# Kernel optimization log

Measured on AMD Instinct MI355X. Metric: run time of the kernel, lower is better.

The kernel has to match this reference:

```python
import jax, jax.numpy as jnp
import numpy as np

ALPHA, BETA, INIT_P = 100.0, 1000.0, 2.0
K_NEIGHBORS = 24


def index_points(pts, idx):
    # pts: [B,N,C], idx: [B,...] int -> [B,...,C]
    B = pts.shape[0]
    b = jnp.arange(B).reshape((B,) + (1,) * (idx.ndim - 1))
    return pts[b, idx]


def fps(xyz, m):
    # furthest point sampling, deterministic start at index 0. xyz: [B,N,3]
    B, N, _ = xyz.shape
    def step(carry, _):
        dist, far = carry
        centroid = xyz[jnp.arange(B), far]              # [B,3]
        d = jnp.sum((xyz - centroid[:, None, :]) ** 2, -1)
        dist = jnp.minimum(dist, d)
        nxt = jnp.argmax(dist, -1).astype(jnp.int32)
        return (dist, nxt), far
    init = (jnp.full((B, N), 1e10, xyz.dtype), jnp.zeros((B,), jnp.int32))
    _, idx = jax.lax.scan(step, init, None, length=m)
    return idx.T                                        # [B,m]


def knn_indices(k, xyz, centers):
    # squared distances [B,G,N], k smallest
    d = (jnp.sum(centers ** 2, -1)[..., None]
         - 2.0 * jnp.einsum('bgc,bnc->bgn', centers, xyz)
         + jnp.sum(xyz ** 2, -1)[:, None, :])
    _, idx = jax.lax.top_k(-d, k)
    return idx                                          # [B,G,K]


def normalize(x, ref):
    # torch: mean = ref.unsqueeze(-2); std over ALL elements of (x-mean), ddof=1
    d = x - ref[..., None, :]
    std = jnp.std(d, ddof=1)
    return d / (std + 1e-5)


def fourier_map(t, Bmat):
    # t: [B,7,G,K]; Bmat: [7, C//2] (already includes scale) -> [B,C,G,K]
    x = jnp.transpose(t, (0, 2, 3, 1))                  # [B,G,K,7]
    proj = 2.0 * jnp.pi * (x @ Bmat)                    # [B,G,K,C/2]
    f = jnp.concatenate([jnp.sin(proj), jnp.cos(proj)], -1)
    f = jnp.sign(f) * jnp.abs(f) ** 5
    return jnp.transpose(f, (0, 3, 1, 2))


def tr_embed(my_dim, t):
    # t: [B,3,G,K] -> [B,my_dim,G,K]
    B, C, G, K = t.shape
    F = my_dim // (2 * C)
    dim_embed = ALPHA ** (jnp.arange(F, dtype=t.dtype) / F)
    div = BETA * t[..., None] / dim_embed               # [B,3,G,K,F]
    pe = jnp.stack([jnp.sin(div), jnp.cos(div)], -1).reshape(B, C, G, K, 2 * F)
    pe = jnp.transpose(pe, (0, 1, 4, 2, 3)).reshape(B, my_dim, G, K)
    return pe


def lga(lc_xyz, lc_x, knn_xyz, knn_x, Bmat):
    B, G, K, C = knn_x.shape
    knn_x = normalize(knn_x, lc_x)
    knn_xyz = normalize(knn_xyz, lc_xyz)
    lc_rep = jnp.transpose(jnp.broadcast_to(lc_xyz[:, :, None, :], (B, G, K, 3)), (0, 3, 1, 2))
    knn_xyz_t = jnp.transpose(knn_xyz, (0, 3, 1, 2))    # [B,3,G,K]
    knn_x_t = jnp.transpose(knn_x, (0, 3, 1, 2))        # [B,C,G,K]
    cross = jnp.cross(knn_xyz_t, lc_rep, axis=1)
    dot = jnp.sum(knn_xyz_t * lc_rep, 1, keepdims=True)
    emb_in = jnp.concatenate([knn_xyz_t, cross, dot], 1)  # [B,7,G,K]
    emb = fourier_map(emb_in, Bmat)                       # [B,C,G,K]
    knn_x_w = jnp.concatenate([knn_x_t, emb], 1)          # [B,2C,G,K]
    pe = tr_embed(2 * C, knn_xyz_t) + tr_embed(2 * C, lc_rep)
    return (knn_x_w + pe) * pe


def k_anp(x):
    # x: [B,2C,G,K], data-dependent p-norm attention over K
    std = jnp.std(x, axis=-1, ddof=1, keepdims=True)
    p = jax.lax.stop_gradient(INIT_P + jnp.log1p(std.mean()))  # torch uses .item()
    norm = jnp.sum(jnp.abs(x) ** p, -1, keepdims=True) ** (1.0 / p)
    lc = norm / (norm + 1e-8)
    e = jnp.exp(lc)
    return (x * e).mean(-1) / e.mean(-1)                # [B,2C,G]


def bn_gelu(x, gamma, beta):
    # BatchNorm1d in training mode (batch stats, biased var) + exact GELU
    mean = x.mean((0, 2), keepdims=True)
    var = ((x - mean) ** 2).mean((0, 2), keepdims=True)
    y = (x - mean) / jnp.sqrt(var + 1e-5) * gamma[None, :, None] + beta[None, :, None]
    return jax.nn.gelu(y, approximate=False)


def stage(xyz, x, group_num, Bmat, gamma, beta):
    # xyz: [B,N,3]; x: [B,C,N]
    feats = jnp.transpose(x, (0, 2, 1))
    fi = fps(xyz, group_num)
    lc_xyz = index_points(xyz, fi)
    lc_x = index_points(feats, fi)
    ki = knn_indices(K_NEIGHBORS, xyz, lc_xyz)
    knn_xyz = index_points(xyz, ki)
    knn_x = index_points(feats, ki)
    w = lga(lc_xyz, lc_x, knn_xyz, knn_x, Bmat)
    pooled = k_anp(w) + w.mean(-1)                      # [B,2C,G]
    return lc_xyz, bn_gelu(pooled, gamma, beta)


def setup_inputs() -> dict:
    key = jax.random.key(0)
    k1, k2, k3, k4 = jax.random.split(key, 4)
    B, N, C0 = 4, 4096, 72
    return {
        'xyz': jax.random.uniform(k1, (B, N, 3), jnp.float32),
        'x': jax.random.normal(k2, (B, C0, N), jnp.float32),
        'fourier_B0': jax.random.normal(k3, (7, C0 // 2), jnp.float32) * 50.0,
        'fourier_B1': jax.random.normal(k4, (7, C0), jnp.float32) * 50.0,
        'bn_gamma0': jnp.ones((2 * C0,), jnp.float32),
        'bn_beta0': jnp.zeros((2 * C0,), jnp.float32),
        'bn_gamma1': jnp.ones((4 * C0,), jnp.float32),
        'bn_beta1': jnp.zeros((4 * C0,), jnp.float32),
    }


def reference(xyz, x, fourier_B0, fourier_B1, bn_gamma0, bn_beta0, bn_gamma1, bn_beta1):
    N = xyz.shape[1]
    xyz, x = stage(xyz, x, N // 2, fourier_B0, bn_gamma0, bn_beta0)   # -> [B,144,2048]
    xyz, x = stage(xyz, x, N // 4, fourier_B1, bn_gamma1, bn_beta1)   # -> [B,288,1024]
    return x
```

## Files before the change

kernel.cpp:

```cpp
#include <hip/hip_runtime.h>
#include <math.h>

#define KNB 24

typedef float v2f __attribute__((ext_vector_type(2)));

template<int CTRL>
__device__ __forceinline__ float dppmax(float v) {
    int t = __builtin_amdgcn_update_dpp(0, __float_as_int(v), CTRL, 0xf, 0xf, true);
    return fmaxf(v, __int_as_float(t));
}
template<int CTRL>
__device__ __forceinline__ unsigned dppmaxu(unsigned v) {
    unsigned t = (unsigned)__builtin_amdgcn_update_dpp(0, (int)v, CTRL, 0xf, 0xf, true);
    return v > t ? v : t;
}

template<int NPT, int NWAVE>
__global__ __launch_bounds__(64 * NWAVE) void k_fps_tr(const float* __restrict__ xyz,
                                                       int* __restrict__ fi,
                                                       int N, int M,
                                                       const float* __restrict__ x0,
                                                       float* __restrict__ feats,
                                                       int C, int NT, int nT, int cT) {
#pragma clang fp contract(off)
    const int NP2 = NPT / 2;
    const int tid = threadIdx.x;
    extern __shared__ char smc[];

    if ((int)blockIdx.x >= gridDim.x - 0 && false) return;

    if ((int)blockIdx.x >= (int)(gridDim.x) ) return;

    if ((int)blockIdx.x >= (int)0 && (int)blockIdx.x >= (int)( 0) && false) return;

    if ((int)blockIdx.x >= (int)( (int)gridDim.x - nT * cT * 4 ) && (int)blockIdx.x >= 4) {
        int bid = blockIdx.x - 4;
        int tilesPerB = nT * cT;
        int b = bid / tilesPerB;
        int t2 = bid - b * tilesPerB;
        int cTile = t2 / nT;
        int nTile = t2 - cTile * nT;
        int tx = tid & 31, ty = tid >> 5;
        float* tile = (float*)smc;
#pragma unroll
        for (int k = 0; k < 4; ++k) {
            int c = cTile * 32 + ty + k * 8, n = nTile * 32 + tx;
            if (c < C && n < NT) tile[(ty + k * 8) * 33 + tx] = x0[((size_t)b * C + c) * NT + n];
        }
        __syncthreads();
#pragma unroll
        for (int k = 0; k < 4; ++k) {
            int n = nTile * 32 + ty + k * 8, c = cTile * 32 + tx;
            if (c < C && n < NT) feats[((size_t)b * NT + n) * C + c] = tile[tx * 33 + ty + k * 8];
        }
        return;
    }

    const int b = blockIdx.x;
    const int lane = tid & 63;
    const int wid = tid >> 6;
    unsigned long long* keys = (unsigned long long*)smc;
    int* fi_lds = (int*)(smc + 2 * NWAVE * 8);
    size_t poff = ((size_t)(2 * NWAVE * 8) + (size_t)M * 4 + 15) & ~(size_t)15;
    float4* pts = (float4*)(smc + poff);

    const float* p = xyz + (size_t)b * N * 3;
    for (int i = tid; i < N; i += 64 * NWAVE)
        pts[i] = make_float4(p[i*3], p[i*3+1], p[i*3+2], 0.0f);
    __syncthreads();

    const int base = tid * NPT;
    v2f rx[NP2], ry[NP2], rz[NP2], dist[NP2];
#pragma unroll
    for (int j = 0; j < NP2; ++j) {
        float4 a = pts[base + 2*j];
        float4 c = pts[base + 2*j + 1];
        rx[j] = (v2f){a.x, c.x}; ry[j] = (v2f){a.y, c.y}; rz[j] = (v2f){a.z, c.z};
        dist[j] = (v2f){1e10f, 1e10f};
    }

    int far = 0;
    float4 cpt = pts[0];
    float cx = cpt.x, cy = cpt.y, cz = cpt.z;
    for (int it = 0; it < M; ++it) {
        if (tid == 0) fi_lds[it] = far;
        v2f cx2 = (v2f){cx, cx}, cy2 = (v2f){cy, cy}, cz2 = (v2f){cz, cz};
        v2f bv2 = (v2f){-1.0f, -1.0f};
#pragma unroll
        for (int j = 0; j < NP2; ++j) {
            v2f dx = rx[j] - cx2, dy = ry[j] - cy2, dz = rz[j] - cz2;
            v2f d = (dx*dx + dy*dy) + dz*dz;
            v2f dd = __builtin_elementwise_min(dist[j], d);
            dist[j] = dd;
            bv2 = __builtin_elementwise_max(bv2, dd);
        }
        float bv = fmaxf(bv2.x, bv2.y);
        int bi = 0;
#pragma unroll
        for (int j = NP2 - 1; j >= 0; --j) {
            if (dist[j].y == bv) bi = base + 2*j + 1;
            if (dist[j].x == bv) bi = base + 2*j;
        }
        float r = bv;
        r = dppmax<0x111>(r); r = dppmax<0x112>(r);
        r = dppmax<0x114>(r); r = dppmax<0x118>(r);
        r = dppmax<0x142>(r); r = dppmax<0x143>(r);
        float wmax = __int_as_float(__builtin_amdgcn_readlane(__float_as_int(r), 63));
        unsigned long long mask = __ballot(bv == wmax);
        int src = __builtin_ctzll(mask);
        int wbi = __builtin_amdgcn_readlane(bi, src);
        unsigned long long key =
            ((unsigned long long)__float_as_uint(wmax) << 32) | (unsigned)(~wbi);
        if (lane == 0) keys[(it & 1) * NWAVE + wid] = key;
        __syncthreads();
        unsigned long long k0 = keys[(it & 1) * NWAVE + 0];
#pragma unroll
        for (int w = 1; w < NWAVE; ++w) {
            unsigned long long kw = keys[(it & 1) * NWAVE + w];
            if (kw > k0) k0 = kw;
        }
        far = (int)(~(unsigned)k0);
        float4 c = pts[far];
        cx = c.x; cy = c.y; cz = c.z;
    }
    __syncthreads();
    for (int i = tid; i < M; i += 64 * NWAVE) fi[b * M + i] = fi_lds[i];
}

template<int NPT>
__global__ __launch_bounds__(256) void k_knn_t(const float* __restrict__ xyz,
                                               const float* __restrict__ feats,
                                               const int* __restrict__ fi,
                                               float* __restrict__ lc_xyz,
                                               float* __restrict__ lc_x,
                                               int* __restrict__ ki,
                                               double* __restrict__ part,
                                               int B, int N, int G, int C, int identity) {
#pragma clang fp contract(off)
    int bg = blockIdx.x; int b = bg / G; int g = bg % G;
    int idx = identity ? g : fi[bg];
    const int tid = threadIdx.x;
    const int lane = tid & 63;
    const int wid = tid >> 6;
    __shared__ unsigned long long keys[2][4];
    __shared__ int kis[KNB];
    __shared__ float cfeat[144];
    const float* p = xyz + (size_t)b * N * 3;
    float cx = p[idx*3], cy = p[idx*3+1], cz = p[idx*3+2];
    if (tid < 3) lc_xyz[(size_t)bg * 3 + tid] = p[idx*3 + tid];
    for (int c = tid; c < C; c += 256) {
        float v = feats[((size_t)b * N + idx) * C + c];
        lc_x[(size_t)bg * C + c] = v;
        cfeat[c] = v;
    }
    float cc = (cx*cx + cy*cy) + cz*cz;
    const int base = tid * NPT;
    float dist[NPT];
#pragma unroll
    for (int j = 0; j < NPT; ++j) {
        float x0 = p[(base+j)*3], x1 = p[(base+j)*3+1], x2 = p[(base+j)*3+2];
        float xx = (x0*x0 + x1*x1) + x2*x2;
        float dt = (cx*x0 + cy*x1) + cz*x2;
        dist[j] = (cc - 2.0f*dt) + xx;
    }
    for (int kk = 0; kk < KNB; ++kk) {
        float bv = 1e30f;
#pragma unroll
        for (int j = 0; j < NPT; ++j) bv = fminf(bv, dist[j]);
        int lj = 0;
#pragma unroll
        for (int j = NPT - 1; j >= 0; --j) if (dist[j] == bv) lj = j;
        unsigned ub = ~__float_as_uint(bv);
        unsigned r = ub;
        r = dppmaxu<0x111>(r); r = dppmaxu<0x112>(r);
        r = dppmaxu<0x114>(r); r = dppmaxu<0x118>(r);
        r = dppmaxu<0x142>(r); r = dppmaxu<0x143>(r);
        unsigned uwin = (unsigned)__builtin_amdgcn_readlane((int)r, 63);
        unsigned long long mask = __ballot(ub == uwin);
        int src = __builtin_ctzll(mask);
        int gi = __builtin_amdgcn_readlane(base + lj, src);
        unsigned long long key = ((unsigned long long)uwin << 32) | (unsigned)(~gi);
        if (lane == 0) keys[kk & 1][wid] = key;
        __syncthreads();
        unsigned long long k0 = keys[kk & 1][0];
#pragma unroll
        for (int w = 1; w < 4; ++w) {
            unsigned long long kw = keys[kk & 1][w];
            if (kw > k0) k0 = kw;
        }
        int win = (int)(~(unsigned)k0);
        if (tid == 0) kis[kk] = win;
        if (win >= base && win < base + NPT) {
            int wj = win - base;
#pragma unroll
            for (int j = 0; j < NPT; ++j) if (j == wj) dist[j] = 1e30f;
        }
    }
    __syncthreads();
    if (tid < KNB) ki[(size_t)bg * KNB + tid] = kis[tid];
    double s = 0.0, s2 = 0.0, s3 = 0.0, s4 = 0.0;
    for (int i = tid; i < KNB * C; i += 256) {
        int k = i / C, c = i - k * C;
        float d = feats[((size_t)b * N + kis[k]) * C + c] - cfeat[c];
        s += (double)d; s2 += (double)d * (double)d;
    }
    if (tid < KNB * 3) {
        int k = tid / 3, c = tid - k * 3;
        float ctr = (c == 0) ? cx : ((c == 1) ? cy : cz);
        float d = p[kis[k] * 3 + c] - ctr;
        s3 += (double)d; s4 += (double)d * (double)d;
    }
    for (int off = 32; off > 0; off >>= 1) {
        s += __shfl_down(s, off); s2 += __shfl_down(s2, off);
        s3 += __shfl_down(s3, off); s4 += __shfl_down(s4, off);
    }
    __shared__ double sw[4][4];
    if ((tid & 63) == 0) {
        sw[wid][0] = s; sw[wid][1] = s2; sw[wid][2] = s3; sw[wid][3] = s4;
    }
    __syncthreads();
    if (tid == 0) {
        double t0 = 0.0, t1 = 0.0, t2 = 0.0, t3 = 0.0;
        for (int w = 0; w < 4; ++w) {
            t0 += sw[w][0]; t1 += sw[w][1]; t2 += sw[w][2]; t3 += sw[w][3];
        }
        double* q = part + (size_t)bg * 4;
        q[0] = t0; q[1] = t1; q[2] = t2; q[3] = t3;
    }
}

__global__ __launch_bounds__(1024) void k_reduce(const double* __restrict__ part,
                                                 double* __restrict__ acc, int n) {
    double s0 = 0.0, s1 = 0.0, s2 = 0.0, s3 = 0.0;
    for (int i = threadIdx.x; i < n; i += 1024) {
        const double* q = part + (size_t)i * 4;
        s0 += q[0]; s1 += q[1]; s2 += q[2]; s3 += q[3];
    }
    for (int off = 32; off > 0; off >>= 1) {
        s0 += __shfl_down(s0, off); s1 += __shfl_down(s1, off);
        s2 += __shfl_down(s2, off); s3 += __shfl_down(s3, off);
    }
    __shared__ double sw[16][4];
    int wid = threadIdx.x >> 6;
    if ((threadIdx.x & 63) == 0) {
        sw[wid][0] = s0; sw[wid][1] = s1; sw[wid][2] = s2; sw[wid][3] = s3;
    }
    __syncthreads();
    if (threadIdx.x == 0) {
        double t0 = 0.0, t1 = 0.0, t2 = 0.0, t3 = 0.0;
        for (int w = 0; w < 16; ++w) {
            t0 += sw[w][0]; t1 += sw[w][1]; t2 += sw[w][2]; t3 += sw[w][3];
        }
        acc[0] = t0; acc[1] = t1; acc[2] = t2; acc[3] = t3;
    }
}

__global__ __launch_bounds__(256) void k_feature(
    const float* __restrict__ xyz, const float* __restrict__ feats,
    const float* __restrict__ lc_xyz, const float* __restrict__ lc_x,
    const int* __restrict__ ki, const float* __restrict__ Bmat,
    const double* __restrict__ accp, float* __restrict__ pooled,
    int B, int N, int G, int C, double nx, double nz)
{
    int bg = blockIdx.x; int b = bg / G; int g = bg % G;
    int tid = threadIdx.x;
    int C2 = C >> 1;
    int Cout = 2 * C;
    int F = C / 3;
    extern __shared__ float sm[];
    float* t7    = sm;
    float* sxyzn = t7 + KNB * 7;
    int*   kidx  = (int*)(sxyzn + KNB * 3);
    float* semb  = (float*)(kidx + KNB);
    float* sfeat = semb + KNB * C;

    double a0 = accp[0], a1 = accp[1], a2 = accp[2], a3 = accp[3];
    double vx = (a1 - a0 * a0 / nx) / (nx - 1.0);
    float invx = 1.0f / (sqrtf((float)vx) + 1e-5f);
    double vz = (a3 - a2 * a2 / nz) / (nz - 1.0);
    float invz = 1.0f / (sqrtf((float)vz) + 1e-5f);

    float l0 = lc_xyz[(size_t)bg*3], l1 = lc_xyz[(size_t)bg*3+1], l2 = lc_xyz[(size_t)bg*3+2];

    if (tid < KNB) {
        int idx = ki[(size_t)bg * KNB + tid];
        kidx[tid] = idx;
        const float* q = xyz + ((size_t)b * N + idx) * 3;
        float a0f = (q[0]-l0)*invz, a1f = (q[1]-l1)*invz, a2f = (q[2]-l2)*invz;
        float c0 = a1f*l2 - a2f*l1;
        float c1 = a2f*l0 - a0f*l2;
        float c2 = a0f*l1 - a1f*l0;
        float dt = (a0f*l0 + a1f*l1) + a2f*l2;
        float* tp = t7 + tid * 7;
        tp[0]=a0f; tp[1]=a1f; tp[2]=a2f; tp[3]=c0; tp[4]=c1; tp[5]=c2; tp[6]=dt;
        sxyzn[tid*3]=a0f; sxyzn[tid*3+1]=a1f; sxyzn[tid*3+2]=a2f;
    }
    __syncthreads();
    for (int i = tid; i < KNB * C; i += blockDim.x) {
        int k = i / C, c = i - k * C;
        sfeat[i] = feats[((size_t)b * N + kidx[k]) * C + c];
    }
    const float TWO_PI = 6.2831854820251465f;
    for (int i = tid; i < KNB * C2; i += blockDim.x) {
        int k = i / C2, m2 = i % C2;
        const float* tp = t7 + k * 7;
        float s = 0.0f;
        for (int j = 0; j < 7; ++j) s += tp[j] * Bmat[j * C2 + m2];
        float pr = TWO_PI * s;
        float sn, cs;
        __sincosf(pr, &sn, &cs);
        float sn2 = sn*sn, cs2 = cs*cs;
        semb[k*C + m2]      = sn2*sn2*sn;
        semb[k*C + C2 + m2] = cs2*cs2*cs;
    }
    __syncthreads();
    for (int m = tid; m < Cout; m += blockDim.x) {
        int c3 = m / (2 * F);
        int r  = m % (2 * F);
        int f  = r >> 1;
        int trig = r & 1;
        float de = __powf(100.0f, (float)f / (float)F);
        float rde = 1000.0f / de;
        float lv = (c3 == 0) ? l0 : ((c3 == 1) ? l1 : l2);
        float a2v = lv * rde;
        float pe2 = trig ? __cosf(a2v) : __sinf(a2v);
        float lfm = (m < C) ? lc_x[(size_t)bg * C + m] : 0.0f;
        float acc = 0.0f;
        for (int k = 0; k < KNB; ++k) {
            float v;
            if (m < C) {
                v = (sfeat[k * C + m] - lfm) * invx;
            } else {
                v = semb[k * C + (m - C)];
            }
            float a1v = sxyzn[k*3 + c3] * rde;
            float pe1 = trig ? __cosf(a1v) : __sinf(a1v);
            float pe = pe1 + pe2;
            acc += (v + pe) * pe;
        }
        float mean = acc / 24.0f;
        pooled[((size_t)b * Cout + m) * G + g] = 2.0f * mean;
    }
}

__global__ __launch_bounds__(256) void k_bn(const float* __restrict__ pooled,
                                            const float* __restrict__ gamma,
                                            const float* __restrict__ beta,
                                            float* __restrict__ out,
                                            int B, int Cout, int G, int transposed) {
    int m = blockIdx.x;
    double s = 0.0, s2 = 0.0;
    for (int i = threadIdx.x; i < B * G; i += 256) {
        int b = i / G, g = i % G;
        float v = pooled[((size_t)b * Cout + m) * G + g];
        s += (double)v; s2 += (double)v * (double)v;
    }
    for (int off = 32; off > 0; off >>= 1) { s += __shfl_down(s, off); s2 += __shfl_down(s2, off); }
    __shared__ double sw[4], sw2[4];
    __shared__ float smv[2];
    int wid = threadIdx.x >> 6;
    if ((threadIdx.x & 63) == 0) { sw[wid] = s; sw2[wid] = s2; }
    __syncthreads();
    if (threadIdx.x == 0) {
        double ts = sw[0] + sw[1] + sw[2] + sw[3];
        double ts2 = sw2[0] + sw2[1] + sw2[2] + sw2[3];
        double n = (double)(B * G);
        double mean = ts / n;
        double var = ts2 / n - mean * mean;
        smv[0] = (float)mean; smv[1] = (float)var;
    }
    __syncthreads();
    float mean = smv[0], var = smv[1];
    float ga = gamma[m], be = beta[m];
    for (int i = threadIdx.x; i < B * G; i += 256) {
        int b = i / G, g = i % G;
        float v = pooled[((size_t)b * Cout + m) * G + g];
        float y = (v - mean) / sqrtf(var + 1e-5f) * ga + be;
        float ge = 0.5f * y * (1.0f + erff(y / 1.4142135381698608f));
        if (transposed) out[((size_t)b * G + g) * Cout + m] = ge;
        else            out[((size_t)b * Cout + m) * G + g] = ge;
    }
}

extern "C" void kernel_launch(void* const* d_in, const int* in_sizes, int n_in,
                              void* d_out, int out_size, void* d_ws, size_t ws_size,
                              hipStream_t stream) {
    const int B = 4, N1 = 4096, C0 = 72, G1 = 2048, Co1 = 144;
    const int N2 = 2048, C1 = 144, G2 = 1024, Co2 = 288;

    const float* xyz = (const float*)d_in[0];
    const float* x0  = (const float*)d_in[1];
    const float* B0  = (const float*)d_in[2];
    const float* B1  = (const float*)d_in[3];
    const float* g0  = (const float*)d_in[4];
    const float* be0 = (const float*)d_in[5];
    const float* g1  = (const float*)d_in[6];
    const float* be1 = (const float*)d_in[7];
    float* out = (float*)d_out;

    char* wp = (char*)d_ws;
    size_t off = 0;
    auto A = [&](size_t bytes) -> void* {
        void* p = wp + off;
        off += (bytes + 255) & ~(size_t)255;
        return p;
    };
    float* feats1  = (float*)A((size_t)B*N1*C0*4);
    int*   fi1     = (int*)  A((size_t)B*G1*4);
    float* lcx1    = (float*)A((size_t)B*G1*3*4);
    float* lcf1    = (float*)A((size_t)B*G1*C0*4);
    int*   ki1     = (int*)  A((size_t)B*G1*KNB*4);
    double* acc    = (double*)A(8*8);
    double* part   = (double*)A((size_t)B*G1*4*8);
    float* pooled1 = (float*)A((size_t)B*Co1*G1*4);
    float* feats2  = (float*)A((size_t)B*N2*C1*4);
    float* lcx2    = (float*)A((size_t)B*G2*3*4);
    float* lcf2    = lcf1;
    int*   ki2     = ki1;
    float* pooled2 = feats1;

    {
        const int nT = N1 / 32, cT = (C0 + 31) / 32;
        size_t poff = ((size_t)(2*4*8) + (size_t)G1*4 + 15) & ~(size_t)15;
        size_t shm = poff + (size_t)N1*16;
        k_fps_tr<16, 4><<<B + B*nT*cT, 256, shm, stream>>>(xyz, fi1, N1, G1,
                                                           x0, feats1, C0, N1, nT, cT);
    }
    k_knn_t<16><<<B*G1, 256, 0, stream>>>(xyz, feats1, fi1, lcx1, lcf1, ki1, part,
                                          B, N1, G1, C0, 0);
    k_reduce<<<1, 1024, 0, stream>>>(part, acc, B*G1);
    {
        size_t shf = (size_t)(KNB*7 + KNB*3 + KNB + 2*KNB*C0) * 4;
        k_feature<<<B*G1, 256, shf, stream>>>(xyz, feats1, lcx1, lcf1, ki1, B0, acc, pooled1,
                                              B, N1, G1, C0,
                                              (double)B*G1*KNB*C0, (double)B*G1*KNB*3);
    }
    k_bn<<<Co1, 256, 0, stream>>>(pooled1, g0, be0, feats2, B, Co1, G1, 1);

    k_knn_t<8><<<B*G2, 256, 0, stream>>>(lcx1, feats2, (const int*)nullptr,
                                         lcx2, lcf2, ki2, part, B, N2, G2, C1, 1);
    k_reduce<<<1, 1024, 0, stream>>>(part, acc + 4, B*G2);
    {
        size_t shf = (size_t)(KNB*7 + KNB*3 + KNB + 2*KNB*C1) * 4;
        k_feature<<<B*G2, 256, shf, stream>>>(lcx1, feats2, lcx2, lcf2, ki2, B1, acc + 4, pooled2,
                                              B, N2, G2, C1,
                                              (double)B*G2*KNB*C1, (double)B*G2*KNB*3);
    }
    k_bn<<<Co2, 256, 0, stream>>>(pooled2, g1, be1, out, B, Co2, G2, 0);
}
```

Before: 1.628 ms.

## Pack FPS distance and index into a double key and widen to eight waves

The FPS argmax now packs each point's float distance and its inverted index into one 64-bit word and reduces it as a double with fmax. This replaces the separate value reduction, equality scan, ballot and readlane with a single DPP max chain. The block grows from four to eight waves with eight points per thread, so each serial iteration has less work per thread but a wider cross-wave reduction. The transpose path is generalized to the new row count. Double-precision max and 64-bit DPP moves cost more per step, and the trick depends on non-negative distances ordering correctly as doubles.

Result: faster. 1.577 ms (-3.1%).

```diff
diff --git a/kernel.cpp b/kernel.cpp
--- a/kernel.cpp
+++ b/kernel.cpp
@@ -15,26 +15,30 @@
     unsigned t = (unsigned)__builtin_amdgcn_update_dpp(0, (int)v, CTRL, 0xf, 0xf, true);
     return v > t ? v : t;
 }
+template<int CTRL>
+__device__ __forceinline__ double dppmax64(double v) {
+    unsigned long long u = __double_as_longlong(v);
+    int lo = (int)(unsigned)(u & 0xffffffffull);
+    int hi = (int)(unsigned)(u >> 32);
+    int tlo = __builtin_amdgcn_update_dpp(0, lo, CTRL, 0xf, 0xf, true);
+    int thi = __builtin_amdgcn_update_dpp(0, hi, CTRL, 0xf, 0xf, true);
+    double t = __longlong_as_double(((unsigned long long)(unsigned)thi << 32) | (unsigned)tlo);
+    return __builtin_fmax(v, t);
+}
 
 template<int NPT, int NWAVE>
-__global__ __launch_bounds__(64 * NWAVE) void k_fps_tr(const float* __restrict__ xyz,
-                                                       int* __restrict__ fi,
-                                                       int N, int M,
-                                                       const float* __restrict__ x0,
-                                                       float* __restrict__ feats,
-                                                       int C, int NT, int nT, int cT) {
+__global__ __launch_bounds__(64 * NWAVE, 1) void k_fps_tr(const float* __restrict__ xyz,
+                                                          int* __restrict__ fi,
+                                                          int N, int M,
+                                                          const float* __restrict__ x0,
+                                                          float* __restrict__ feats,
+                                                          int C, int NT, int nT, int cT) {
 #pragma clang fp contract(off)
     const int NP2 = NPT / 2;
     const int tid = threadIdx.x;
     extern __shared__ char smc[];
 
-    if ((int)blockIdx.x >= gridDim.x - 0 && false) return;
-
-    if ((int)blockIdx.x >= (int)(gridDim.x) ) return;
-
-    if ((int)blockIdx.x >= (int)0 && (int)blockIdx.x >= (int)( 0) && false) return;
-
-    if ((int)blockIdx.x >= (int)( (int)gridDim.x - nT * cT * 4 ) && (int)blockIdx.x >= 4) {
+    if ((int)blockIdx.x >= 4) {
         int bid = blockIdx.x - 4;
         int tilesPerB = nT * cT;
         int b = bid / tilesPerB;
@@ -42,17 +46,16 @@
         int cTile = t2 / nT;
         int nTile = t2 - cTile * nT;
         int tx = tid & 31, ty = tid >> 5;
+        const int ROWS = 2 * NWAVE;
         float* tile = (float*)smc;
-#pragma unroll
-        for (int k = 0; k < 4; ++k) {
-            int c = cTile * 32 + ty + k * 8, n = nTile * 32 + tx;
-            if (c < C && n < NT) tile[(ty + k * 8) * 33 + tx] = x0[((size_t)b * C + c) * NT + n];
+        for (int r = ty; r < 32; r += ROWS) {
+            int c = cTile * 32 + r, n = nTile * 32 + tx;
+            if (c < C && n < NT) tile[r * 33 + tx] = x0[((size_t)b * C + c) * NT + n];
         }
         __syncthreads();
-#pragma unroll
-        for (int k = 0; k < 4; ++k) {
-            int n = nTile * 32 + ty + k * 8, c = cTile * 32 + tx;
-            if (c < C && n < NT) feats[((size_t)b * NT + n) * C + c] = tile[tx * 33 + ty + k * 8];
+        for (int r = ty; r < 32; r += ROWS) {
+            int n = nTile * 32 + r, c = cTile * 32 + tx;
+            if (c < C && n < NT) feats[((size_t)b * NT + n) * C + c] = tile[tx * 33 + r];
         }
         return;
     }
@@ -72,12 +75,15 @@
 
     const int base = tid * NPT;
     v2f rx[NP2], ry[NP2], rz[NP2], dist[NP2];
+    unsigned lowc[NPT];
 #pragma unroll
     for (int j = 0; j < NP2; ++j) {
         float4 a = pts[base + 2*j];
         float4 c = pts[base + 2*j + 1];
         rx[j] = (v2f){a.x, c.x}; ry[j] = (v2f){a.y, c.y}; rz[j] = (v2f){a.z, c.z};
         dist[j] = (v2f){1e10f, 1e10f};
+        lowc[2*j]   = ~(unsigned)(base + 2*j);
+        lowc[2*j+1] = ~(unsigned)(base + 2*j + 1);
     }
 
     int far = 0;
@@ -86,41 +92,43 @@
     for (int it = 0; it < M; ++it) {
         if (tid == 0) fi_lds[it] = far;
         v2f cx2 = (v2f){cx, cx}, cy2 = (v2f){cy, cy}, cz2 = (v2f){cz, cz};
-        v2f bv2 = (v2f){-1.0f, -1.0f};
+        double kA = 0.0, kB = 0.0;
 #pragma unroll
         for (int j = 0; j < NP2; ++j) {
             v2f dx = rx[j] - cx2, dy = ry[j] - cy2, dz = rz[j] - cz2;
             v2f d = (dx*dx + dy*dy) + dz*dz;
             v2f dd = __builtin_elementwise_min(dist[j], d);
             dist[j] = dd;
-            bv2 = __builtin_elementwise_max(bv2, dd);
-        }
-        float bv = fmaxf(bv2.x, bv2.y);
-        int bi = 0;
-#pragma unroll
-        for (int j = NP2 - 1; j >= 0; --j) {
-            if (dist[j].y == bv) bi = base + 2*j + 1;
-            if (dist[j].x == bv) bi = base + 2*j;
-        }
-        float r = bv;
-        r = dppmax<0x111>(r); r = dppmax<0x112>(r);
-        r = dppmax<0x114>(r); r = dppmax<0x118>(r);
-        r = dppmax<0x142>(r); r = dppmax<0x143>(r);
-        float wmax = __int_as_float(__builtin_amdgcn_readlane(__float_as_int(r), 63));
-        unsigned long long mask = __ballot(bv == wmax);
-        int src = __builtin_ctzll(mask);
-        int wbi = __builtin_amdgcn_readlane(bi, src);
-        unsigned long long key =
-            ((unsigned long long)__float_as_uint(wmax) << 32) | (unsigned)(~wbi);
-        if (lane == 0) keys[(it & 1) * NWAVE + wid] = key;
+            double k0 = __longlong_as_double(
+                ((unsigned long long)__float_as_uint(dd.x) << 32) | lowc[2*j]);
+            double k1 = __longlong_as_double(
+                ((unsigned long long)__float_as_uint(dd.y) << 32) | lowc[2*j+1]);
+            kA = __builtin_fmax(kA, k0);
+            kB = __builtin_fmax(kB, k1);
+        }
+        double km = __builtin_fmax(kA, kB);
+        km = dppmax64<0x111>(km); km = dppmax64<0x112>(km);
+        km = dppmax64<0x114>(km); km = dppmax64<0x118>(km);
+        km = dppmax64<0x142>(km); km = dppmax64<0x143>(km);
+        if (lane == 63) keys[(it & 1) * NWAVE + wid] = __double_as_longlong(km);
         __syncthreads();
-        unsigned long long k0 = keys[(it & 1) * NWAVE + 0];
-#pragma unroll
-        for (int w = 1; w < NWAVE; ++w) {
-            unsigned long long kw = keys[(it & 1) * NWAVE + w];
-            if (kw > k0) k0 = kw;
-        }
-        far = (int)(~(unsigned)k0);
+        const unsigned long long* kk = keys + (it & 1) * NWAVE;
+        double g;
+        if (NWAVE == 8) {
+            double m0 = __builtin_fmax(__longlong_as_double(kk[0]), __longlong_as_double(kk[1]));
+            double m1 = __builtin_fmax(__longlong_as_double(kk[2]), __longlong_as_double(kk[3]));
+            double m2 = __builtin_fmax(__longlong_as_double(kk[4]), __longlong_as_double(kk[5]));
+            double m3 = __builtin_fmax(__longlong_as_double(kk[6]), __longlong_as_double(kk[7]));
+            m0 = __builtin_fmax(m0, m1);
+            m2 = __builtin_fmax(m2, m3);
+            g = __builtin_fmax(m0, m2);
+        } else {
+            g = __longlong_as_double(kk[0]);
+#pragma unroll
+            for (int w = 1; w < NWAVE; ++w)
+                g = __builtin_fmax(g, __longlong_as_double(kk[w]));
+        }
+        far = (int)(~(unsigned)__double_as_longlong(g));
         float4 c = pts[far];
         cx = c.x; cy = c.y; cz = c.z;
     }
@@ -422,10 +430,11 @@
 
     {
         const int nT = N1 / 32, cT = (C0 + 31) / 32;
-        size_t poff = ((size_t)(2*4*8) + (size_t)G1*4 + 15) & ~(size_t)15;
+        const int NW = 8;
+        size_t poff = ((size_t)(2*NW*8) + (size_t)G1*4 + 15) & ~(size_t)15;
         size_t shm = poff + (size_t)N1*16;
-        k_fps_tr<16, 4><<<B + B*nT*cT, 256, shm, stream>>>(xyz, fi1, N1, G1,
-                                                           x0, feats1, C0, N1, nT, cT);
+        k_fps_tr<8, NW><<<B + B*nT*cT, 64*NW, shm, stream>>>(xyz, fi1, N1, G1,
+                                                             x0, feats1, C0, N1, nT, cT);
     }
     k_knn_t<16><<<B*G1, 256, 0, stream>>>(xyz, feats1, fi1, lcx1, lcf1, ki1, part,
                                           B, N1, G1, C0, 0);
```

## Broadcast winning point coordinates via wave reduction instead of LDS point cache in FPS

Applied to the files above, without the earlier changes.

The FPS kernel no longer stages all points in shared memory. Each wave's winner now publishes its coordinates next to its key, and every thread runs a tree reduction over the per-wave candidates, which removes the dependent LDS load of the chosen point from each iteration. The block grows from 4 to 8 waves with 8 points per thread, so each thread carries half as many registers and the per-iteration work is spread more widely. The costs are a larger cross-wave reduction per step and per-lane selects to extract the winning coordinates. The transpose tiles are generalised to handle any wave count.

New measurement: 2.588 ms. 1.59x slower.

```diff
diff --git a/kernel.cpp b/kernel.cpp
--- a/kernel.cpp
+++ b/kernel.cpp
@@ -17,24 +17,18 @@
 }
 
 template<int NPT, int NWAVE>
-__global__ __launch_bounds__(64 * NWAVE) void k_fps_tr(const float* __restrict__ xyz,
-                                                       int* __restrict__ fi,
-                                                       int N, int M,
-                                                       const float* __restrict__ x0,
-                                                       float* __restrict__ feats,
-                                                       int C, int NT, int nT, int cT) {
+__global__ __launch_bounds__(64 * NWAVE, 1) void k_fps_tr(const float* __restrict__ xyz,
+                                                          int* __restrict__ fi,
+                                                          int N, int M,
+                                                          const float* __restrict__ x0,
+                                                          float* __restrict__ feats,
+                                                          int C, int NT, int nT, int cT) {
 #pragma clang fp contract(off)
     const int NP2 = NPT / 2;
     const int tid = threadIdx.x;
     extern __shared__ char smc[];
 
-    if ((int)blockIdx.x >= gridDim.x - 0 && false) return;
-
-    if ((int)blockIdx.x >= (int)(gridDim.x) ) return;
-
-    if ((int)blockIdx.x >= (int)0 && (int)blockIdx.x >= (int)( 0) && false) return;
-
-    if ((int)blockIdx.x >= (int)( (int)gridDim.x - nT * cT * 4 ) && (int)blockIdx.x >= 4) {
+    if ((int)blockIdx.x >= 4) {
         int bid = blockIdx.x - 4;
         int tilesPerB = nT * cT;
         int b = bid / tilesPerB;
@@ -42,17 +36,16 @@
         int cTile = t2 / nT;
         int nTile = t2 - cTile * nT;
         int tx = tid & 31, ty = tid >> 5;
+        const int ROWS = 2 * NWAVE;
         float* tile = (float*)smc;
-#pragma unroll
-        for (int k = 0; k < 4; ++k) {
-            int c = cTile * 32 + ty + k * 8, n = nTile * 32 + tx;
-            if (c < C && n < NT) tile[(ty + k * 8) * 33 + tx] = x0[((size_t)b * C + c) * NT + n];
+        for (int r = ty; r < 32; r += ROWS) {
+            int c = cTile * 32 + r, n = nTile * 32 + tx;
+            if (c < C && n < NT) tile[r * 33 + tx] = x0[((size_t)b * C + c) * NT + n];
         }
         __syncthreads();
-#pragma unroll
-        for (int k = 0; k < 4; ++k) {
-            int n = nTile * 32 + ty + k * 8, c = cTile * 32 + tx;
-            if (c < C && n < NT) feats[((size_t)b * NT + n) * C + c] = tile[tx * 33 + ty + k * 8];
+        for (int r = ty; r < 32; r += ROWS) {
+            int n = nTile * 32 + r, c = cTile * 32 + tx;
+            if (c < C && n < NT) feats[((size_t)b * NT + n) * C + c] = tile[tx * 33 + r];
         }
         return;
     }
@@ -61,28 +54,23 @@
     const int lane = tid & 63;
     const int wid = tid >> 6;
     unsigned long long* keys = (unsigned long long*)smc;
-    int* fi_lds = (int*)(smc + 2 * NWAVE * 8);
-    size_t poff = ((size_t)(2 * NWAVE * 8) + (size_t)M * 4 + 15) & ~(size_t)15;
-    float4* pts = (float4*)(smc + poff);
+    float4* wco = (float4*)(smc + 2 * NWAVE * 8);
+    int* fi_lds = (int*)(smc + 2 * NWAVE * 8 + 2 * NWAVE * 16);
 
     const float* p = xyz + (size_t)b * N * 3;
-    for (int i = tid; i < N; i += 64 * NWAVE)
-        pts[i] = make_float4(p[i*3], p[i*3+1], p[i*3+2], 0.0f);
-    __syncthreads();
-
     const int base = tid * NPT;
     v2f rx[NP2], ry[NP2], rz[NP2], dist[NP2];
 #pragma unroll
     for (int j = 0; j < NP2; ++j) {
-        float4 a = pts[base + 2*j];
-        float4 c = pts[base + 2*j + 1];
-        rx[j] = (v2f){a.x, c.x}; ry[j] = (v2f){a.y, c.y}; rz[j] = (v2f){a.z, c.z};
+        int i0 = base + 2 * j, i1 = base + 2 * j + 1;
+        rx[j] = (v2f){p[i0*3],   p[i1*3]};
+        ry[j] = (v2f){p[i0*3+1], p[i1*3+1]};
+        rz[j] = (v2f){p[i0*3+2], p[i1*3+2]};
         dist[j] = (v2f){1e10f, 1e10f};
     }
 
     int far = 0;
-    float4 cpt = pts[0];
-    float cx = cpt.x, cy = cpt.y, cz = cpt.z;
+    float cx = p[0], cy = p[1], cz = p[2];
     for (int it = 0; it < M; ++it) {
         if (tid == 0) fi_lds[it] = far;
         v2f cx2 = (v2f){cx, cx}, cy2 = (v2f){cy, cy}, cz2 = (v2f){cz, cz};
@@ -96,11 +84,17 @@
             bv2 = __builtin_elementwise_max(bv2, dd);
         }
         float bv = fmaxf(bv2.x, bv2.y);
-        int bi = 0;
+        int lj = 0;
 #pragma unroll
         for (int j = NP2 - 1; j >= 0; --j) {
-            if (dist[j].y == bv) bi = base + 2*j + 1;
-            if (dist[j].x == bv) bi = base + 2*j;
+            if (dist[j].y == bv) lj = 2*j + 1;
+            if (dist[j].x == bv) lj = 2*j;
+        }
+        float sx = rx[0].x, sy = ry[0].x, sz = rz[0].x;
+#pragma unroll
+        for (int j = 0; j < NP2; ++j) {
+            if (lj == 2*j)     { sx = rx[j].x; sy = ry[j].x; sz = rz[j].x; }
+            if (lj == 2*j + 1) { sx = rx[j].y; sy = ry[j].y; sz = rz[j].y; }
         }
         float r = bv;
         r = dppmax<0x111>(r); r = dppmax<0x112>(r);
@@ -109,20 +103,37 @@
         float wmax = __int_as_float(__builtin_amdgcn_readlane(__float_as_int(r), 63));
         unsigned long long mask = __ballot(bv == wmax);
         int src = __builtin_ctzll(mask);
-        int wbi = __builtin_amdgcn_readlane(bi, src);
-        unsigned long long key =
-            ((unsigned long long)__float_as_uint(wmax) << 32) | (unsigned)(~wbi);
-        if (lane == 0) keys[(it & 1) * NWAVE + wid] = key;
+        int widx = __builtin_amdgcn_readlane(base + lj, src);
+        float wx = __int_as_float(__builtin_amdgcn_readlane(__float_as_int(sx), src));
+        float wy = __int_as_float(__builtin_amdgcn_readlane(__float_as_int(sy), src));
+        float wz = __int_as_float(__builtin_amdgcn_readlane(__float_as_int(sz), src));
+        if (lane == 0) {
+            keys[(it & 1) * NWAVE + wid] =
+                ((unsigned long long)__float_as_uint(wmax) << 32) | (unsigned)(~widx);
+            wco[(it & 1) * NWAVE + wid] = make_float4(wx, wy, wz, 0.0f);
+        }
         __syncthreads();
-        unsigned long long k0 = keys[(it & 1) * NWAVE + 0];
-#pragma unroll
-        for (int w = 1; w < NWAVE; ++w) {
-            unsigned long long kw = keys[(it & 1) * NWAVE + w];
-            if (kw > k0) k0 = kw;
-        }
-        far = (int)(~(unsigned)k0);
-        float4 c = pts[far];
-        cx = c.x; cy = c.y; cz = c.z;
+        const unsigned long long* kk = keys + (it & 1) * NWAVE;
+        const float4* cc = wco + (it & 1) * NWAVE;
+        double kt[NWAVE]; float xt[NWAVE], yt[NWAVE], zt[NWAVE];
+#pragma unroll
+        for (int w = 0; w < NWAVE; ++w) {
+            kt[w] = __longlong_as_double((long long)kk[w]);
+            float4 c4 = cc[w];
+            xt[w] = c4.x; yt[w] = c4.y; zt[w] = c4.z;
+        }
+#pragma unroll
+        for (int sft = 1; sft < NWAVE; sft <<= 1) {
+#pragma unroll
+            for (int w = 0; w + sft < NWAVE; w += 2 * sft) {
+                if (kt[w + sft] > kt[w]) {
+                    kt[w] = kt[w + sft];
+                    xt[w] = xt[w + sft]; yt[w] = yt[w + sft]; zt[w] = zt[w + sft];
+                }
+            }
+        }
+        far = (int)(~(unsigned)__double_as_longlong(kt[0]));
+        cx = xt[0]; cy = yt[0]; cz = zt[0];
     }
     __syncthreads();
     for (int i = tid; i < M; i += 64 * NWAVE) fi[b * M + i] = fi_lds[i];
@@ -422,10 +433,10 @@
 
     {
         const int nT = N1 / 32, cT = (C0 + 31) / 32;
-        size_t poff = ((size_t)(2*4*8) + (size_t)G1*4 + 15) & ~(size_t)15;
-        size_t shm = poff + (size_t)N1*16;
-        k_fps_tr<16, 4><<<B + B*nT*cT, 256, shm, stream>>>(xyz, fi1, N1, G1,
-                                                           x0, feats1, C0, N1, nT, cT);
+        const int NW = 8;
+        size_t shm = (size_t)(2*NW*8) + (size_t)(2*NW*16) + (size_t)G1*4;
+        k_fps_tr<8, NW><<<B + B*nT*cT, 64*NW, shm, stream>>>(xyz, fi1, N1, G1,
+                                                             x0, feats1, C0, N1, nT, cT);
     }
     k_knn_t<16><<<B*G1, 256, 0, stream>>>(xyz, feats1, fi1, lcx1, lcf1, ki1, part,
                                           B, N1, G1, C0, 0);
```
